# Kernel optimization log

Measured on AMD Instinct MI355X. Metric: run time of the kernel, lower is better.

The kernel has to match this reference:

```python
import jax, jax.numpy as jnp
import numpy as np

N_LAYERS, H, D, DH = 4, 16, 1024, 64
V_FR, V_EN = 32000, 32000
L_FR, L_EN, B = 513, 512, 2


def _pos_enc(x):
    # x: [L, B, D]; pe[i,j] = sin(i/10000^(j/D)) if j even else cos(i/10000^((j-1)/D))
    L, _, D_ = x.shape
    pos = jnp.arange(L, dtype=jnp.float32)[:, None]
    j = jnp.arange(D_)
    ang = pos / jnp.power(10000.0, (j - (j % 2)).astype(jnp.float32) / D_)
    pe = jnp.where(j % 2 == 0, jnp.sin(ang), jnp.cos(ang))
    return x + pe[:, None, :]


def _ln(x, g, b):
    mu = jnp.mean(x, -1, keepdims=True)
    var = jnp.mean((x - mu) ** 2, -1, keepdims=True)
    return (x - mu) * jax.lax.rsqrt(var + 1e-5) * g + b


def _mha(q_in, k_in, v_in, w, bias, causal):
    # w: [3, H, D, dh], bias: [3, H, dh]
    dh = w.shape[-1]
    Q = jnp.einsum('bld,hde->bhle', q_in, w[0]) + bias[0][None, :, None, :]
    K = jnp.einsum('bmd,hde->bhme', k_in, w[1]) + bias[1][None, :, None, :]
    V = jnp.einsum('bmd,hde->bhme', v_in, w[2]) + bias[2][None, :, None, :]
    s = jnp.einsum('bhle,bhme->bhlm', Q, K) / jnp.sqrt(jnp.float32(dh))
    if causal:
        m = jnp.tril(jnp.ones((s.shape[-2], s.shape[-1]), bool))
        s = jnp.where(m, s, -jnp.inf)
    a = jax.nn.softmax(s, axis=-1)
    o = jnp.einsum('bhlm,bhme->bhle', a, V)
    b_, h_, l_, dh_ = o.shape
    return o.transpose(0, 2, 1, 3).reshape(b_, l_, h_ * dh_)


def setup_inputs() -> dict:
    key = jax.random.key(0)
    ks = jax.random.split(key, 24)
    s = 0.02
    rn = lambda k, shp: jax.random.normal(k, shp, jnp.float32) * s
    return {
        'fr': jax.random.randint(ks[0], (L_FR, B), 0, V_FR),
        'en': jax.random.randint(ks[1], (L_EN, B), 0, V_EN),
        'emb_fr': rn(ks[2], (V_FR, D)),
        'emb_en': rn(ks[3], (V_EN, D)),
        'enc_qkv_w': rn(ks[4], (N_LAYERS, 3, H, D, DH)),
        'enc_qkv_b': rn(ks[5], (N_LAYERS, 3, H, DH)),
        'enc_fc1_w': rn(ks[6], (N_LAYERS, D, D)),
        'enc_fc1_b': rn(ks[7], (N_LAYERS, D)),
        'enc_fc2_w': rn(ks[8], (N_LAYERS, D, D)),
        'enc_fc2_b': rn(ks[9], (N_LAYERS, D)),
        'enc_ln_g': jnp.ones((N_LAYERS, 2, D)) + rn(ks[10], (N_LAYERS, 2, D)),
        'enc_ln_b': rn(ks[11], (N_LAYERS, 2, D)),
        'dec_self_qkv_w': rn(ks[12], (N_LAYERS, 3, H, D, DH)),
        'dec_self_qkv_b': rn(ks[13], (N_LAYERS, 3, H, DH)),
        'dec_cross_qkv_w': rn(ks[14], (N_LAYERS, 3, H, D, DH)),
        'dec_cross_qkv_b': rn(ks[15], (N_LAYERS, 3, H, DH)),
        'dec_fc1_w': rn(ks[16], (N_LAYERS, D, D)),
        'dec_fc1_b': rn(ks[17], (N_LAYERS, D)),
        'dec_fc2_w': rn(ks[18], (N_LAYERS, D, D)),
        'dec_fc2_b': rn(ks[19], (N_LAYERS, D)),
        'dec_ln_g': jnp.ones((N_LAYERS, 3, D)) + rn(ks[20], (N_LAYERS, 3, D)),
        'dec_ln_b': rn(ks[21], (N_LAYERS, 3, D)),
        'out_w': rn(ks[22], (D, V_EN)),
        'out_b': rn(ks[23], (V_EN,)),
    }


def reference(fr, en, emb_fr, emb_en, enc_qkv_w, enc_qkv_b, enc_fc1_w, enc_fc1_b,
              enc_fc2_w, enc_fc2_b, enc_ln_g, enc_ln_b, dec_self_qkv_w,
              dec_self_qkv_b, dec_cross_qkv_w, dec_cross_qkv_b, dec_fc1_w,
              dec_fc1_b, dec_fc2_w, dec_fc2_b, dec_ln_g, dec_ln_b, out_w, out_b):
    # Encoder (dropout p=0 -> identity in eval math)
    x = _pos_enc(emb_fr[fr[1:]]).transpose(1, 0, 2)  # [B, L_src, D]
    for n in range(N_LAYERS):
        a = _mha(x, x, x, enc_qkv_w[n], enc_qkv_b[n], causal=False)
        x = _ln(x + a, enc_ln_g[n, 0], enc_ln_b[n, 0])
        h = jnp.maximum(x @ enc_fc1_w[n] + enc_fc1_b[n], 0.0) @ enc_fc2_w[n] + enc_fc2_b[n]
        x = _ln(x + h, enc_ln_g[n, 1], enc_ln_b[n, 1])
    enc_out = x
    # Decoder
    y = _pos_enc(emb_en[en]).transpose(1, 0, 2)  # [B, L_tgt, D]
    for n in range(N_LAYERS):
        a = _mha(y, y, y, dec_self_qkv_w[n], dec_self_qkv_b[n], causal=True)
        y = _ln(y + a, dec_ln_g[n, 0], dec_ln_b[n, 0])
        c = _mha(y, enc_out, enc_out, dec_cross_qkv_w[n], dec_cross_qkv_b[n], causal=False)
        y = _ln(y + c, dec_ln_g[n, 1], dec_ln_b[n, 1])
        h = jnp.maximum(y @ dec_fc1_w[n] + dec_fc1_b[n], 0.0) @ dec_fc2_w[n] + dec_fc2_b[n]
        y = _ln(y + h, dec_ln_g[n, 2], dec_ln_b[n, 2])
    return y @ out_w + out_b  # [B, L_tgt, V_EN]
```

## Files before the change

kernel.cpp:

```cpp
#include <hip/hip_runtime.h>
#include <stdint.h>
#include <stddef.h>

typedef unsigned short u16;
typedef __attribute__((ext_vector_type(8))) short bf16x8;
typedef __attribute__((ext_vector_type(4))) float f32x4;

#define DEV __device__ __forceinline__

DEV float b2f(u16 u) { union { float f; uint32_t i; } v; v.i = ((uint32_t)u) << 16; return v.f; }
DEV u16 f2b(float f) {
  uint32_t x = __float_as_uint(f);
  x += 0x7fffu + ((x >> 16) & 1u);
  return (u16)(x >> 16);
}
DEV bf16x8 ld8f(const float* f) {
  float4 a = *(const float4*)f;
  float4 b = *(const float4*)(f + 4);
  bf16x8 r;
  ((u16*)&r)[0] = f2b(a.x); ((u16*)&r)[1] = f2b(a.y);
  ((u16*)&r)[2] = f2b(a.z); ((u16*)&r)[3] = f2b(a.w);
  ((u16*)&r)[4] = f2b(b.x); ((u16*)&r)[5] = f2b(b.y);
  ((u16*)&r)[6] = f2b(b.z); ((u16*)&r)[7] = f2b(b.w);
  return r;
}
DEV void gload16(const u16* g, u16* l) {
  __builtin_amdgcn_global_load_lds((const __attribute__((address_space(1))) void*)g,
                                   (__attribute__((address_space(3))) void*)l, 16, 0, 0);
}
DEV f32x4 mfma16(bf16x8 a, bf16x8 b, f32x4 c) {
  return __builtin_amdgcn_mfma_f32_16x16x32_bf16(a, b, c, 0, 0, 0);
}

__global__ __launch_bounds__(256) void transpose_w(const float* __restrict__ src,
                                                   u16* __restrict__ dst, int K, int N) {
  __shared__ u16 t[32][33];
  int tx = threadIdx.x, ty = threadIdx.y;
  int k0 = blockIdx.x * 32, n0 = blockIdx.y * 32;
  size_t base = (size_t)blockIdx.z * K * N;
#pragma unroll
  for (int i = 0; i < 4; i++) {
    int k = ty + 8 * i;
    t[k][tx] = f2b(src[base + (size_t)(k0 + k) * N + n0 + tx]);
  }
  __syncthreads();
#pragma unroll
  for (int i = 0; i < 4; i++) {
    int n = ty + 8 * i;
    dst[base + (size_t)(n0 + n) * K + k0 + tx] = t[tx][n];
  }
}

__global__ __launch_bounds__(256) void embed_k(const int* __restrict__ tok, const float* __restrict__ emb,
                                               float* __restrict__ o32, u16* __restrict__ ob, int shift) {
  int row = blockIdx.x;
  int b = row >> 9, l = row & 511;
  int tk = tok[(size_t)(l + shift) * 2 + b];
  const float* e = emb + (size_t)tk * 1024;
  const float c0 = -9.210340371976184f / 1024.f;
#pragma unroll
  for (int i = 0; i < 4; i++) {
    int d = threadIdx.x + i * 256;
    int j2 = d & ~1;
    float ang = (float)l * expf(c0 * (float)j2);
    float pe = (d & 1) ? cosf(ang) : sinf(ang);
    float rv = e[d] + pe;
    o32[(size_t)row * 1024 + d] = rv;
    ob[(size_t)row * 1024 + d] = f2b(rv);
  }
}

__global__ __launch_bounds__(256) void ln_k(const float* d,
                                            const float* __restrict__ g, const float* __restrict__ bb,
                                            float* o32, u16* __restrict__ ob) {
  int row = blockIdx.x;
  int tid = threadIdx.x;
  const float4 dv = ((const float4*)(d + (size_t)row * 1024))[tid];
  float v[4] = {dv.x, dv.y, dv.z, dv.w};
  float s = 0.f, s2 = 0.f;
#pragma unroll
  for (int i = 0; i < 4; i++) { s += v[i]; s2 += v[i] * v[i]; }
#pragma unroll
  for (int off = 1; off < 64; off <<= 1) {
    s += __shfl_xor(s, off);
    s2 += __shfl_xor(s2, off);
  }
  __shared__ float red[8];
  int wid = tid >> 6;
  if ((tid & 63) == 0) { red[wid * 2] = s; red[wid * 2 + 1] = s2; }
  __syncthreads();
  s = red[0] + red[2] + red[4] + red[6];
  s2 = red[1] + red[3] + red[5] + red[7];
  float mu = s * (1.f / 1024.f);
  float var = s2 * (1.f / 1024.f) - mu * mu;
  float inv = rsqrtf(var + 1e-5f);
  const float4 gv = ((const float4*)g)[tid];
  const float4 bv = ((const float4*)bb)[tid];
  float4 ov;
  ov.x = (v[0] - mu) * inv * gv.x + bv.x;
  ov.y = (v[1] - mu) * inv * gv.y + bv.y;
  ov.z = (v[2] - mu) * inv * gv.z + bv.z;
  ov.w = (v[3] - mu) * inv * gv.w + bv.w;
  ((float4*)(o32 + (size_t)row * 1024))[tid] = ov;
  uint2 p;
  p.x = (uint32_t)f2b(ov.x) | ((uint32_t)f2b(ov.y) << 16);
  p.y = (uint32_t)f2b(ov.z) | ((uint32_t)f2b(ov.w) << 16);
  ((uint2*)(ob + (size_t)row * 1024))[tid] = p;
}

template <bool RELU>
__global__ __launch_bounds__(256) void gemm_fc(const u16* __restrict__ A, const u16* __restrict__ BT,
                                               const float* __restrict__ bias,
                                               const float* __restrict__ resid, void* __restrict__ out,
                                               int N, int K) {
  __shared__ __align__(16) u16 lA[2][64 * 32];
  __shared__ __align__(16) u16 lB[2][64 * 32];
  int bx = blockIdx.x, by = blockIdx.y;
  int tid = threadIdx.x, lane = tid & 63, wid = tid >> 6;
  int l15 = lane & 15, lg = lane >> 4;
  int bm = by * 64, bn = bx * 64;
  int wr = (wid >> 1) * 32, wc = (wid & 1) * 32;
  f32x4 acc[2][2] = {};
  int r_s = tid >> 2, c_s = tid & 3;
  for (int kt = 0; kt < K; kt += 64) {
    __syncthreads();
#pragma unroll
    for (int s = 0; s < 2; s++) {
      gload16(A + (size_t)(bm + r_s) * K + kt + s * 32 + c_s * 8, &lA[s][(size_t)(wid * 64) * 8]);
      gload16(BT + (size_t)(bn + r_s) * K + kt + s * 32 + c_s * 8, &lB[s][(size_t)(wid * 64) * 8]);
    }
    __syncthreads();
#pragma unroll
    for (int s = 0; s < 2; s++) {
      bf16x8 af[2], bf_[2];
#pragma unroll
      for (int m = 0; m < 2; m++) af[m] = *(const bf16x8*)&lA[s][(wr + m * 16 + l15) * 32 + lg * 8];
#pragma unroll
      for (int n = 0; n < 2; n++) bf_[n] = *(const bf16x8*)&lB[s][(wc + n * 16 + l15) * 32 + lg * 8];
#pragma unroll
      for (int m = 0; m < 2; m++)
#pragma unroll
        for (int n = 0; n < 2; n++) acc[m][n] = mfma16(af[m], bf_[n], acc[m][n]);
    }
  }
#pragma unroll
  for (int n = 0; n < 2; n++) {
    int col = bn + wc + n * 16 + l15;
    float bv = bias[col];
#pragma unroll
    for (int m = 0; m < 2; m++) {
#pragma unroll
      for (int r = 0; r < 4; r++) {
        int row = bm + wr + m * 16 + lg * 4 + r;
        float v = acc[m][n][r] + bv;
        if (RELU) ((u16*)out)[(size_t)row * N + col] = f2b(fmaxf(v, 0.f));
        else ((float*)out)[(size_t)row * N + col] = v + resid[(size_t)row * N + col];
      }
    }
  }
}

__global__ __launch_bounds__(256) void gemm_qkv3(const u16* __restrict__ Aq, const u16* __restrict__ Akv,
                                                 const u16* __restrict__ WT, const float* __restrict__ bias,
                                                 u16* __restrict__ Qo, u16* __restrict__ Ko,
                                                 u16* __restrict__ Vto) {
  __shared__ __align__(16) u16 lA[2][64 * 32];
  __shared__ __align__(16) u16 lB[2][64 * 32];
  int bx = blockIdx.x, by = blockIdx.y;
  int t = bx >> 4;
  const u16* A = (t == 0) ? Aq : Akv;
  int tid = threadIdx.x, lane = tid & 63, wid = tid >> 6;
  int l15 = lane & 15, lg = lane >> 4;
  int bm = by * 64, bn = bx * 64;
  int wr = (wid >> 1) * 32, wc = (wid & 1) * 32;
  f32x4 acc[2][2] = {};
  int r_s = tid >> 2, c_s = tid & 3;
  for (int kt = 0; kt < 1024; kt += 64) {
    __syncthreads();
#pragma unroll
    for (int s = 0; s < 2; s++) {
      gload16(A + (size_t)(bm + r_s) * 1024 + kt + s * 32 + c_s * 8, &lA[s][(size_t)(wid * 64) * 8]);
      gload16(WT + (size_t)(bn + r_s) * 1024 + kt + s * 32 + c_s * 8, &lB[s][(size_t)(wid * 64) * 8]);
    }
    __syncthreads();
#pragma unroll
    for (int s = 0; s < 2; s++) {
      bf16x8 af[2], bf_[2];
#pragma unroll
      for (int m = 0; m < 2; m++) af[m] = *(const bf16x8*)&lA[s][(wr + m * 16 + l15) * 32 + lg * 8];
#pragma unroll
      for (int n = 0; n < 2; n++) bf_[n] = *(const bf16x8*)&lB[s][(wc + n * 16 + l15) * 32 + lg * 8];
#pragma unroll
      for (int m = 0; m < 2; m++)
#pragma unroll
        for (int n = 0; n < 2; n++) acc[m][n] = mfma16(af[m], bf_[n], acc[m][n]);
    }
  }
#pragma unroll
  for (int n = 0; n < 2; n++) {
    int col = bn + wc + n * 16 + l15;
    int h = (col >> 6) & 15, e = col & 63;
    float bv = bias[col];
#pragma unroll
    for (int m = 0; m < 2; m++) {
#pragma unroll
      for (int r = 0; r < 4; r++) {
        int row = bm + wr + m * 16 + lg * 4 + r;
        int b = row >> 9, l = row & 511;
        u16 vbv = f2b(acc[m][n][r] + bv);
        size_t bhead = (size_t)b * 16 + h;
        if (t == 0) Qo[(bhead * 512 + l) * 64 + e] = vbv;
        else if (t == 1) Ko[(bhead * 512 + l) * 64 + e] = vbv;
        else Vto[(bhead * 64 + e) * 512 + l] = vbv;
      }
    }
  }
}

template <int BM, int BN, int RS, int RM>
__global__ __launch_bounds__(256) void gemm_p3(const u16* __restrict__ A, const u16* __restrict__ BT,
                                               const float* __restrict__ bias, float* __restrict__ out,
                                               int N, int K) {
  constexpr int FM = BM / 32, FN = BN / 32;
  constexpr int L = BM / 64 + BN / 64;
  __shared__ __align__(16) u16 lA[3][BM * 32];
  __shared__ __align__(16) u16 lB[3][BN * 32];
  int b = blockIdx.x;
  int p = (b & 7) + 8 * (b >> RS);
  if (p >= N / BN) return;
  int bx = p, by = (b >> 3) & RM;
  int tid = threadIdx.x, lane = tid & 63, wid = tid >> 6;
  int l15 = lane & 15, lg = lane >> 4;
  int bm = by * BM, bn = bx * BN;
  int wr = (wid >> 1) * (BM / 2), wc = (wid & 1) * (BN / 2);
  f32x4 acc[FM][FN] = {};
  int r_s = tid >> 2, c_s = tid & 3;
  auto stage = [&](int buf, int kt) {
#pragma unroll
    for (int i = 0; i < BM / 64; i++)
      gload16(A + (size_t)(bm + i * 64 + r_s) * K + kt + c_s * 8, &lA[buf][(i * 256 + wid * 64) * 8]);
#pragma unroll
    for (int i = 0; i < BN / 64; i++)
      gload16(BT + (size_t)(bn + i * 64 + r_s) * K + kt + c_s * 8, &lB[buf][(i * 256 + wid * 64) * 8]);
  };
  int nt = K >> 5;
  stage(0, 0);
  stage(1, 32);
  asm volatile("s_waitcnt vmcnt(%0)" ::"n"(L) : "memory");
  __builtin_amdgcn_s_barrier();
  int cur = 0;
  for (int t = 0; t < nt; t++) {
    if (t + 2 < nt) stage(cur == 0 ? 2 : cur - 1, (t + 2) * 32);
    bf16x8 af[FM], bf_[FN];
#pragma unroll
    for (int m = 0; m < FM; m++) af[m] = *(const bf16x8*)&lA[cur][(wr + m * 16 + l15) * 32 + lg * 8];
#pragma unroll
    for (int n = 0; n < FN; n++) bf_[n] = *(const bf16x8*)&lB[cur][(wc + n * 16 + l15) * 32 + lg * 8];
#pragma unroll
    for (int m = 0; m < FM; m++)
#pragma unroll
      for (int n = 0; n < FN; n++) acc[m][n] = mfma16(af[m], bf_[n], acc[m][n]);
    if (t + 2 < nt) {
      asm volatile("s_waitcnt vmcnt(%0)" ::"n"(L) : "memory");
    } else if (t + 1 < nt) {
      asm volatile("s_waitcnt vmcnt(0)" ::: "memory");
    }
    if (t + 1 < nt) __builtin_amdgcn_s_barrier();
    cur = (cur == 2) ? 0 : cur + 1;
  }
#pragma unroll
  for (int n = 0; n < FN; n++) {
    int col = bn + wc + n * 16 + l15;
    float bv = bias[col];
#pragma unroll
    for (int m = 0; m < FM; m++) {
#pragma unroll
      for (int r = 0; r < 4; r++) {
        int row = bm + wr + m * 16 + lg * 4 + r;
        out[(size_t)row * N + col] = acc[m][n][r] + bv;
      }
    }
  }
}

__global__ __launch_bounds__(256) void gemm_bn(const u16* __restrict__ A, const float* __restrict__ B,
                                               const float* __restrict__ bias, float* __restrict__ out,
                                               int N, int K) {
  __shared__ __align__(16) u16 lA[128 * 32];
  __shared__ __align__(16) u16 lBn[32 * 128];
  int b = blockIdx.x;
  int p = (b & 7) + 8 * (b >> 6);
  if (p >= N / 128) return;
  int by = (b >> 3) & 7;
  int tid = threadIdx.x, lane = tid & 63;
  int wid = tid >> 6;
  int l15 = lane & 15, lg = lane >> 4;
  int bm = by * 128, bn = p * 128;
  int wr = (wid >> 1) * 64, wc = (wid & 1) * 64;
  f32x4 acc[4][4] = {};
  int r_s = tid >> 2, c_s = tid & 3;
  int br = tid >> 4, bc = tid & 15;
  for (int kt = 0; kt < K; kt += 32) {
    bf16x8 va[2], vb[2];
#pragma unroll
    for (int it = 0; it < 2; it++) {
      va[it] = *(const bf16x8*)&A[(size_t)(bm + it * 64 + r_s) * K + kt + c_s * 8];
      vb[it] = ld8f(B + (size_t)(kt + it * 16 + br) * N + bn + bc * 8);
    }
    __syncthreads();
#pragma unroll
    for (int it = 0; it < 2; it++) {
      *(bf16x8*)&lA[(size_t)(it * 256 + tid) * 8] = va[it];
      *(bf16x8*)&lBn[(size_t)(it * 256 + tid) * 8] = vb[it];
    }
    __syncthreads();
    bf16x8 af[4], bfr[4];
#pragma unroll
    for (int m = 0; m < 4; m++) af[m] = *(const bf16x8*)&lA[(wr + m * 16 + l15) * 32 + lg * 8];
#pragma unroll
    for (int n = 0; n < 4; n++) {
#pragma unroll
      for (int j = 0; j < 8; j++)
        ((short*)&bfr[n])[j] = (short)lBn[(lg * 8 + j) * 128 + wc + n * 16 + l15];
    }
#pragma unroll
    for (int m = 0; m < 4; m++)
#pragma unroll
      for (int n = 0; n < 4; n++) acc[m][n] = mfma16(af[m], bfr[n], acc[m][n]);
  }
#pragma unroll
  for (int n = 0; n < 4; n++) {
    int col = bn + wc + n * 16 + l15;
    float bv = bias[col];
#pragma unroll
    for (int m = 0; m < 4; m++) {
#pragma unroll
      for (int r = 0; r < 4; r++) {
        int row = bm + wr + m * 16 + lg * 4 + r;
        out[(size_t)row * N + col] = acc[m][n][r] + bv;
      }
    }
  }
}

template <bool CAUSAL>
__global__ __launch_bounds__(256) void attn_k(const u16* __restrict__ Qb, const u16* __restrict__ Kb,
                                              const u16* __restrict__ Vtb, const float* __restrict__ R,
                                              float* __restrict__ Ob) {
  int bh = blockIdx.y;
  int tid = threadIdx.x, lane = tid & 63, w = tid >> 6;
  int l15 = lane & 15, lg = lane >> 4;
  int q0 = blockIdx.x * 64 + w * 16;
  const u16* Qh = Qb + (size_t)bh * 512 * 64;
  const u16* Kh = Kb + (size_t)bh * 512 * 64;
  const u16* Vh = Vtb + (size_t)bh * 64 * 512;
  __shared__ __align__(16) u16 P[4][16 * 40];
  u16* Pw = &P[w][0];
  bf16x8 qa0 = *(const bf16x8*)&Qh[(size_t)(q0 + l15) * 64 + lg * 8];
  bf16x8 qa1 = *(const bf16x8*)&Qh[(size_t)(q0 + l15) * 64 + 32 + lg * 8];
  f32x4 acc[4];
#pragma unroll
  for (int c = 0; c < 4; c++) acc[c] = (f32x4){0.f, 0.f, 0.f, 0.f};
  float ls[4] = {0.f, 0.f, 0.f, 0.f};
  int ktend = CAUSAL ? ((q0 + 15) >> 5) : 15;
  for (int kt = 0; kt <= ktend; kt++) {
    int kv = kt * 32;
    f32x4 z = (f32x4){0.f, 0.f, 0.f, 0.f};
    bf16x8 k00 = *(const bf16x8*)&Kh[(size_t)(kv + l15) * 64 + lg * 8];
    bf16x8 k01 = *(const bf16x8*)&Kh[(size_t)(kv + l15) * 64 + 32 + lg * 8];
    f32x4 s0 = mfma16(qa0, k00, z);
    s0 = mfma16(qa1, k01, s0);
    bf16x8 k10 = *(const bf16x8*)&Kh[(size_t)(kv + 16 + l15) * 64 + lg * 8];
    bf16x8 k11 = *(const bf16x8*)&Kh[(size_t)(kv + 16 + l15) * 64 + 32 + lg * 8];
    f32x4 s1 = mfma16(qa0, k10, z);
    s1 = mfma16(qa1, k11, s1);
#pragma unroll
    for (int r = 0; r < 4; r++) {
      float a0 = s0[r] * 0.125f, a1 = s1[r] * 0.125f;
      if (CAUSAL) {
        int rowg = q0 + lg * 4 + r;
        if (kv + l15 > rowg) a0 = -1e30f;
        if (kv + 16 + l15 > rowg) a1 = -1e30f;
      }
      float p0 = __expf(a0), p1 = __expf(a1);
      ls[r] += p0 + p1;
      int prow = lg * 4 + r;
      Pw[prow * 40 + l15] = f2b(p0);
      Pw[prow * 40 + 16 + l15] = f2b(p1);
    }
    bf16x8 pa = *(const bf16x8*)&Pw[l15 * 40 + lg * 8];
#pragma unroll
    for (int c = 0; c < 4; c++) {
      bf16x8 vb = *(const bf16x8*)&Vh[(size_t)(c * 16 + l15) * 512 + kv + lg * 8];
      acc[c] = mfma16(pa, vb, acc[c]);
    }
  }
#pragma unroll
  for (int r = 0; r < 4; r++) {
#pragma unroll
    for (int off = 1; off < 16; off <<= 1) ls[r] += __shfl_xor(ls[r], off);
  }
  int b = bh >> 4, h = bh & 15;
#pragma unroll
  for (int r = 0; r < 4; r++) {
    float inv = 1.f / ls[r];
    int rowg = q0 + lg * 4 + r;
    size_t off0 = (size_t)(b * 512 + rowg) * 1024 + h * 64;
#pragma unroll
    for (int c = 0; c < 4; c++)
      Ob[off0 + c * 16 + l15] = R[off0 + c * 16 + l15] + acc[c][r] * inv;
  }
}

extern "C" void kernel_launch(void* const* d_in, const int* in_sizes, int n_in,
                              void* d_out, int out_size, void* d_ws, size_t ws_size,
                              hipStream_t stream) {
  const int* fr = (const int*)d_in[0];
  const int* en = (const int*)d_in[1];
  const float* emb_fr = (const float*)d_in[2];
  const float* emb_en = (const float*)d_in[3];
  const float* enc_qkv_w = (const float*)d_in[4];
  const float* enc_qkv_b = (const float*)d_in[5];
  const float* enc_fc1_w = (const float*)d_in[6];
  const float* enc_fc1_b = (const float*)d_in[7];
  const float* enc_fc2_w = (const float*)d_in[8];
  const float* enc_fc2_b = (const float*)d_in[9];
  const float* enc_ln_g = (const float*)d_in[10];
  const float* enc_ln_bb = (const float*)d_in[11];
  const float* dec_self_qkv_w = (const float*)d_in[12];
  const float* dec_self_qkv_b = (const float*)d_in[13];
  const float* dec_cross_qkv_w = (const float*)d_in[14];
  const float* dec_cross_qkv_b = (const float*)d_in[15];
  const float* dec_fc1_w = (const float*)d_in[16];
  const float* dec_fc1_b = (const float*)d_in[17];
  const float* dec_fc2_w = (const float*)d_in[18];
  const float* dec_fc2_b = (const float*)d_in[19];
  const float* dec_ln_g = (const float*)d_in[20];
  const float* dec_ln_bb = (const float*)d_in[21];
  const float* out_w = (const float*)d_in[22];
  const float* out_b = (const float*)d_in[23];

  char* o8 = (char*)d_out;
  u16* qkvT_d = (u16*)o8;
  u16* fcT_d = (u16*)(o8 + 6291456);
  float* x32 = (float*)(o8 + 8388608);
  float* y32 = (float*)(o8 + 12582912);
  float* d32 = (float*)(o8 + 16777216);
  u16* xb = (u16*)(o8 + 20971520);
  u16* hb = (u16*)(o8 + 23068672);
  u16* Qb = (u16*)(o8 + 25165824);
  u16* Kb = (u16*)(o8 + 27262976);
  u16* Vtb = (u16*)(o8 + 29360128);

  char* w8 = (char*)d_ws;
  u16* yb = (u16*)w8;
  u16* outwT = (u16*)(w8 + 2097152);
  u16* eqkvT = (u16*)(w8 + 67633152);
  u16* dsqkvT = (u16*)(w8 + 92798976);
  u16* dcqkvT = (u16*)(w8 + 117964800);
  u16* efc1T = (u16*)(w8 + 143130624);
  u16* efc2T = (u16*)(w8 + 151519232);
  u16* dfc1T = (u16*)(w8 + 159907840);
  u16* dfc2T = (u16*)(w8 + 168296448);
  int tier = (ws_size >= 176685056u) ? 2 : (ws_size >= 67633152u) ? 1 : 0;

  dim3 tb(32, 8);
  if (tier >= 1)
    transpose_w<<<dim3(32, 1000, 1), tb, 0, stream>>>(out_w, outwT, 1024, 32000);
  if (tier == 2) {
    transpose_w<<<dim3(32, 2, 192), tb, 0, stream>>>(enc_qkv_w, eqkvT, 1024, 64);
    transpose_w<<<dim3(32, 2, 192), tb, 0, stream>>>(dec_self_qkv_w, dsqkvT, 1024, 64);
    transpose_w<<<dim3(32, 2, 192), tb, 0, stream>>>(dec_cross_qkv_w, dcqkvT, 1024, 64);
    transpose_w<<<dim3(32, 32, 4), tb, 0, stream>>>(enc_fc1_w, efc1T, 1024, 1024);
    transpose_w<<<dim3(32, 32, 4), tb, 0, stream>>>(enc_fc2_w, efc2T, 1024, 1024);
    transpose_w<<<dim3(32, 32, 4), tb, 0, stream>>>(dec_fc1_w, dfc1T, 1024, 1024);
    transpose_w<<<dim3(32, 32, 4), tb, 0, stream>>>(dec_fc2_w, dfc2T, 1024, 1024);
  }

  embed_k<<<1024, 256, 0, stream>>>(fr, emb_fr, x32, xb, 1);
  embed_k<<<1024, 256, 0, stream>>>(en, emb_en, y32, yb, 0);

  for (int n = 0; n < 4; n++) {
    const u16* wqkv;
    if (tier == 2) wqkv = eqkvT + (size_t)n * 3145728;
    else {
      transpose_w<<<dim3(32, 2, 48), tb, 0, stream>>>(enc_qkv_w + (size_t)n * 48 * 65536, qkvT_d, 1024, 64);
      wqkv = qkvT_d;
    }
    gemm_qkv3<<<dim3(48, 16), 256, 0, stream>>>(xb, xb, wqkv, enc_qkv_b + (size_t)n * 3072, Qb, Kb, Vtb);
    attn_k<false><<<dim3(8, 32), 256, 0, stream>>>(Qb, Kb, Vtb, x32, d32);
    ln_k<<<1024, 256, 0, stream>>>(d32, enc_ln_g + (size_t)(n * 2) * 1024,
                                   enc_ln_bb + (size_t)(n * 2) * 1024, x32, xb);
    const u16* w1;
    if (tier == 2) w1 = efc1T + (size_t)n * 1048576;
    else {
      transpose_w<<<dim3(32, 32, 1), tb, 0, stream>>>(enc_fc1_w + (size_t)n * 1048576, fcT_d, 1024, 1024);
      w1 = fcT_d;
    }
    gemm_fc<true><<<dim3(16, 16), 256, 0, stream>>>(xb, w1, enc_fc1_b + (size_t)n * 1024,
                                                    nullptr, hb, 1024, 1024);
    const u16* w2;
    if (tier == 2) w2 = efc2T + (size_t)n * 1048576;
    else {
      transpose_w<<<dim3(32, 32, 1), tb, 0, stream>>>(enc_fc2_w + (size_t)n * 1048576, fcT_d, 1024, 1024);
      w2 = fcT_d;
    }
    gemm_fc<false><<<dim3(16, 16), 256, 0, stream>>>(hb, w2, enc_fc2_b + (size_t)n * 1024,
                                                     x32, d32, 1024, 1024);
    ln_k<<<1024, 256, 0, stream>>>(d32, enc_ln_g + (size_t)(n * 2 + 1) * 1024,
                                   enc_ln_bb + (size_t)(n * 2 + 1) * 1024, x32, xb);
  }
  for (int n = 0; n < 4; n++) {
    const u16* wq;
    if (tier == 2) wq = dsqkvT + (size_t)n * 3145728;
    else {
      transpose_w<<<dim3(32, 2, 48), tb, 0, stream>>>(dec_self_qkv_w + (size_t)n * 48 * 65536, qkvT_d, 1024, 64);
      wq = qkvT_d;
    }
    gemm_qkv3<<<dim3(48, 16), 256, 0, stream>>>(yb, yb, wq, dec_self_qkv_b + (size_t)n * 3072, Qb, Kb, Vtb);
    attn_k<true><<<dim3(8, 32), 256, 0, stream>>>(Qb, Kb, Vtb, y32, d32);
    ln_k<<<1024, 256, 0, stream>>>(d32, dec_ln_g + (size_t)(n * 3) * 1024,
                                   dec_ln_bb + (size_t)(n * 3) * 1024, y32, yb);
    if (tier == 2) wq = dcqkvT + (size_t)n * 3145728;
    else {
      transpose_w<<<dim3(32, 2, 48), tb, 0, stream>>>(dec_cross_qkv_w + (size_t)n * 48 * 65536, qkvT_d, 1024, 64);
      wq = qkvT_d;
    }
    gemm_qkv3<<<dim3(48, 16), 256, 0, stream>>>(yb, xb, wq, dec_cross_qkv_b + (size_t)n * 3072, Qb, Kb, Vtb);
    attn_k<false><<<dim3(8, 32), 256, 0, stream>>>(Qb, Kb, Vtb, y32, d32);
    ln_k<<<1024, 256, 0, stream>>>(d32, dec_ln_g + (size_t)(n * 3 + 1) * 1024,
                                   dec_ln_bb + (size_t)(n * 3 + 1) * 1024, y32, yb);
    const u16* w1;
    if (tier == 2) w1 = dfc1T + (size_t)n * 1048576;
    else {
      transpose_w<<<dim3(32, 32, 1), tb, 0, stream>>>(dec_fc1_w + (size_t)n * 1048576, fcT_d, 1024, 1024);
      w1 = fcT_d;
    }
    gemm_fc<true><<<dim3(16, 16), 256, 0, stream>>>(yb, w1, dec_fc1_b + (size_t)n * 1024,
                                                    nullptr, hb, 1024, 1024);
    const u16* w2;
    if (tier == 2) w2 = dfc2T + (size_t)n * 1048576;
    else {
      transpose_w<<<dim3(32, 32, 1), tb, 0, stream>>>(dec_fc2_w + (size_t)n * 1048576, fcT_d, 1024, 1024);
      w2 = fcT_d;
    }
    gemm_fc<false><<<dim3(16, 16), 256, 0, stream>>>(hb, w2, dec_fc2_b + (size_t)n * 1024,
                                                     y32, d32, 1024, 1024);
    ln_k<<<1024, 256, 0, stream>>>(d32, dec_ln_g + (size_t)(n * 3 + 2) * 1024,
                                   dec_ln_bb + (size_t)(n * 3 + 2) * 1024, y32, yb);
  }
  if (tier >= 1)
    gemm_p3<128, 128, 6, 7><<<dim3(2048), 256, 0, stream>>>(yb, outwT, out_b, (float*)d_out, 32000, 1024);
  else
    gemm_bn<<<dim3(2048), 256, 0, stream>>>(yb, out_w, out_b, (float*)d_out, 32000, 1024);
}
```

Measured before the change: 991.0 us.

## Double-buffer GEMM LDS loads, prefetch K in attention, merge weight transposes

The fc and qkv GEMMs now double-buffer their LDS tiles and issue the next K-tile's async loads before computing the current one, waiting with vmcnt and raw barriers in place of two syncthreads per iteration. This is meant to hide global-load latency behind the MFMA work. The attention kernel prefetches the next K block into registers. The seven per-weight transpose launches collapse into two batched kernels, relying on the workspace buffers being contiguous. Shared memory use doubles, which may lower occupancy, and the vmcnt(4) count must match the number of outstanding loads per stage.

```diff
diff --git a/kernel.cpp b/kernel.cpp
--- a/kernel.cpp
+++ b/kernel.cpp
@@ -48,6 +48,56 @@
   for (int i = 0; i < 4; i++) {
     int n = ty + 8 * i;
     dst[base + (size_t)(n0 + n) * K + k0 + tx] = t[tx][n];
+  }
+}
+
+__global__ __launch_bounds__(256) void transpose_qkvT(const float* __restrict__ s0,
+                                                      const float* __restrict__ s1,
+                                                      const float* __restrict__ s2,
+                                                      u16* __restrict__ dst) {
+  int z = blockIdx.z;
+  const float* src = (z < 192) ? s0 : (z < 384) ? s1 : s2;
+  int zi = (z < 192) ? z : (z < 384) ? z - 192 : z - 384;
+  size_t sbase = (size_t)zi * 65536;
+  size_t dbase = (size_t)z * 65536;
+  __shared__ u16 t[32][33];
+  int tx = threadIdx.x, ty = threadIdx.y;
+  int k0 = blockIdx.x * 32, n0 = blockIdx.y * 32;
+#pragma unroll
+  for (int i = 0; i < 4; i++) {
+    int k = ty + 8 * i;
+    t[k][tx] = f2b(src[sbase + (size_t)(k0 + k) * 64 + n0 + tx]);
+  }
+  __syncthreads();
+#pragma unroll
+  for (int i = 0; i < 4; i++) {
+    int n = ty + 8 * i;
+    dst[dbase + (size_t)(n0 + n) * 1024 + k0 + tx] = t[tx][n];
+  }
+}
+
+__global__ __launch_bounds__(256) void transpose_fcT(const float* __restrict__ s0,
+                                                     const float* __restrict__ s1,
+                                                     const float* __restrict__ s2,
+                                                     const float* __restrict__ s3,
+                                                     u16* __restrict__ dst) {
+  int z = blockIdx.z;
+  const float* src = (z < 4) ? s0 : (z < 8) ? s1 : (z < 12) ? s2 : s3;
+  size_t sbase = (size_t)(z & 3) * 1048576;
+  size_t dbase = (size_t)z * 1048576;
+  __shared__ u16 t[32][33];
+  int tx = threadIdx.x, ty = threadIdx.y;
+  int k0 = blockIdx.x * 32, n0 = blockIdx.y * 32;
+#pragma unroll
+  for (int i = 0; i < 4; i++) {
+    int k = ty + 8 * i;
+    t[k][tx] = f2b(src[sbase + (size_t)(k0 + k) * 1024 + n0 + tx]);
+  }
+  __syncthreads();
+#pragma unroll
+  for (int i = 0; i < 4; i++) {
+    int n = ty + 8 * i;
+    dst[dbase + (size_t)(n0 + n) * 1024 + k0 + tx] = t[tx][n];
   }
 }
 
@@ -113,8 +163,8 @@
                                                const float* __restrict__ bias,
                                                const float* __restrict__ resid, void* __restrict__ out,
                                                int N, int K) {
-  __shared__ __align__(16) u16 lA[2][64 * 32];
-  __shared__ __align__(16) u16 lB[2][64 * 32];
+  __shared__ __align__(16) u16 lA[2][2][64 * 32];
+  __shared__ __align__(16) u16 lB[2][2][64 * 32];
   int bx = blockIdx.x, by = blockIdx.y;
   int tid = threadIdx.x, lane = tid & 63, wid = tid >> 6;
   int l15 = lane & 15, lg = lane >> 4;
@@ -122,26 +172,38 @@
   int wr = (wid >> 1) * 32, wc = (wid & 1) * 32;
   f32x4 acc[2][2] = {};
   int r_s = tid >> 2, c_s = tid & 3;
-  for (int kt = 0; kt < K; kt += 64) {
-    __syncthreads();
+  auto stage = [&](int pp, int kt) {
 #pragma unroll
     for (int s = 0; s < 2; s++) {
-      gload16(A + (size_t)(bm + r_s) * K + kt + s * 32 + c_s * 8, &lA[s][(size_t)(wid * 64) * 8]);
-      gload16(BT + (size_t)(bn + r_s) * K + kt + s * 32 + c_s * 8, &lB[s][(size_t)(wid * 64) * 8]);
-    }
-    __syncthreads();
+      gload16(A + (size_t)(bm + r_s) * K + kt + s * 32 + c_s * 8, &lA[pp][s][(size_t)(wid * 64) * 8]);
+      gload16(BT + (size_t)(bn + r_s) * K + kt + s * 32 + c_s * 8, &lB[pp][s][(size_t)(wid * 64) * 8]);
+    }
+  };
+  int nt = K >> 6;
+  stage(0, 0);
+  int pp = 0;
+  for (int t = 0; t < nt; t++) {
+    if (t + 1 < nt) {
+      stage(pp ^ 1, (t + 1) * 64);
+      asm volatile("s_waitcnt vmcnt(4)" ::: "memory");
+    } else {
+      asm volatile("s_waitcnt vmcnt(0)" ::: "memory");
+    }
+    __builtin_amdgcn_s_barrier();
 #pragma unroll
     for (int s = 0; s < 2; s++) {
       bf16x8 af[2], bf_[2];
 #pragma unroll
-      for (int m = 0; m < 2; m++) af[m] = *(const bf16x8*)&lA[s][(wr + m * 16 + l15) * 32 + lg * 8];
-#pragma unroll
-      for (int n = 0; n < 2; n++) bf_[n] = *(const bf16x8*)&lB[s][(wc + n * 16 + l15) * 32 + lg * 8];
+      for (int m = 0; m < 2; m++) af[m] = *(const bf16x8*)&lA[pp][s][(wr + m * 16 + l15) * 32 + lg * 8];
+#pragma unroll
+      for (int n = 0; n < 2; n++) bf_[n] = *(const bf16x8*)&lB[pp][s][(wc + n * 16 + l15) * 32 + lg * 8];
 #pragma unroll
       for (int m = 0; m < 2; m++)
 #pragma unroll
         for (int n = 0; n < 2; n++) acc[m][n] = mfma16(af[m], bf_[n], acc[m][n]);
     }
+    __builtin_amdgcn_s_barrier();
+    pp ^= 1;
   }
 #pragma unroll
   for (int n = 0; n < 2; n++) {
@@ -164,37 +226,48 @@
                                                  const u16* __restrict__ WT, const float* __restrict__ bias,
                                                  u16* __restrict__ Qo, u16* __restrict__ Ko,
                                                  u16* __restrict__ Vto) {
-  __shared__ __align__(16) u16 lA[2][64 * 32];
-  __shared__ __align__(16) u16 lB[2][64 * 32];
+  __shared__ __align__(16) u16 lA[2][2][64 * 32];
+  __shared__ __align__(16) u16 lB[2][2][64 * 32];
   int bx = blockIdx.x, by = blockIdx.y;
-  int t = bx >> 4;
-  const u16* A = (t == 0) ? Aq : Akv;
+  int t_ = bx >> 4;
+  const u16* A = (t_ == 0) ? Aq : Akv;
   int tid = threadIdx.x, lane = tid & 63, wid = tid >> 6;
   int l15 = lane & 15, lg = lane >> 4;
   int bm = by * 64, bn = bx * 64;
   int wr = (wid >> 1) * 32, wc = (wid & 1) * 32;
   f32x4 acc[2][2] = {};
   int r_s = tid >> 2, c_s = tid & 3;
-  for (int kt = 0; kt < 1024; kt += 64) {
-    __syncthreads();
+  auto stage = [&](int pp, int kt) {
 #pragma unroll
     for (int s = 0; s < 2; s++) {
-      gload16(A + (size_t)(bm + r_s) * 1024 + kt + s * 32 + c_s * 8, &lA[s][(size_t)(wid * 64) * 8]);
-      gload16(WT + (size_t)(bn + r_s) * 1024 + kt + s * 32 + c_s * 8, &lB[s][(size_t)(wid * 64) * 8]);
-    }
-    __syncthreads();
+      gload16(A + (size_t)(bm + r_s) * 1024 + kt + s * 32 + c_s * 8, &lA[pp][s][(size_t)(wid * 64) * 8]);
+      gload16(WT + (size_t)(bn + r_s) * 1024 + kt + s * 32 + c_s * 8, &lB[pp][s][(size_t)(wid * 64) * 8]);
+    }
+  };
+  stage(0, 0);
+  int pp = 0;
+  for (int t = 0; t < 16; t++) {
+    if (t + 1 < 16) {
+      stage(pp ^ 1, (t + 1) * 64);
+      asm volatile("s_waitcnt vmcnt(4)" ::: "memory");
+    } else {
+      asm volatile("s_waitcnt vmcnt(0)" ::: "memory");
+    }
+    __builtin_amdgcn_s_barrier();
 #pragma unroll
     for (int s = 0; s < 2; s++) {
       bf16x8 af[2], bf_[2];
 #pragma unroll
-      for (int m = 0; m < 2; m++) af[m] = *(const bf16x8*)&lA[s][(wr + m * 16 + l15) * 32 + lg * 8];
-#pragma unroll
-      for (int n = 0; n < 2; n++) bf_[n] = *(const bf16x8*)&lB[s][(wc + n * 16 + l15) * 32 + lg * 8];
+      for (int m = 0; m < 2; m++) af[m] = *(const bf16x8*)&lA[pp][s][(wr + m * 16 + l15) * 32 + lg * 8];
+#pragma unroll
+      for (int n = 0; n < 2; n++) bf_[n] = *(const bf16x8*)&lB[pp][s][(wc + n * 16 + l15) * 32 + lg * 8];
 #pragma unroll
       for (int m = 0; m < 2; m++)
 #pragma unroll
         for (int n = 0; n < 2; n++) acc[m][n] = mfma16(af[m], bf_[n], acc[m][n]);
     }
+    __builtin_amdgcn_s_barrier();
+    pp ^= 1;
   }
 #pragma unroll
   for (int n = 0; n < 2; n++) {
@@ -209,8 +282,8 @@
         int b = row >> 9, l = row & 511;
         u16 vbv = f2b(acc[m][n][r] + bv);
         size_t bhead = (size_t)b * 16 + h;
-        if (t == 0) Qo[(bhead * 512 + l) * 64 + e] = vbv;
-        else if (t == 1) Ko[(bhead * 512 + l) * 64 + e] = vbv;
+        if (t_ == 0) Qo[(bhead * 512 + l) * 64 + e] = vbv;
+        else if (t_ == 1) Ko[(bhead * 512 + l) * 64 + e] = vbv;
         else Vto[(bhead * 64 + e) * 512 + l] = vbv;
       }
     }
@@ -363,17 +436,25 @@
   for (int c = 0; c < 4; c++) acc[c] = (f32x4){0.f, 0.f, 0.f, 0.f};
   float ls[4] = {0.f, 0.f, 0.f, 0.f};
   int ktend = CAUSAL ? ((q0 + 15) >> 5) : 15;
+  bf16x8 kn00 = *(const bf16x8*)&Kh[(size_t)(l15) * 64 + lg * 8];
+  bf16x8 kn01 = *(const bf16x8*)&Kh[(size_t)(l15) * 64 + 32 + lg * 8];
+  bf16x8 kn10 = *(const bf16x8*)&Kh[(size_t)(16 + l15) * 64 + lg * 8];
+  bf16x8 kn11 = *(const bf16x8*)&Kh[(size_t)(16 + l15) * 64 + 32 + lg * 8];
   for (int kt = 0; kt <= ktend; kt++) {
     int kv = kt * 32;
+    bf16x8 c00 = kn00, c01 = kn01, c10 = kn10, c11 = kn11;
+    if (kt < ktend) {
+      int kv2 = kv + 32;
+      kn00 = *(const bf16x8*)&Kh[(size_t)(kv2 + l15) * 64 + lg * 8];
+      kn01 = *(const bf16x8*)&Kh[(size_t)(kv2 + l15) * 64 + 32 + lg * 8];
+      kn10 = *(const bf16x8*)&Kh[(size_t)(kv2 + 16 + l15) * 64 + lg * 8];
+      kn11 = *(const bf16x8*)&Kh[(size_t)(kv2 + 16 + l15) * 64 + 32 + lg * 8];
+    }
     f32x4 z = (f32x4){0.f, 0.f, 0.f, 0.f};
-    bf16x8 k00 = *(const bf16x8*)&Kh[(size_t)(kv + l15) * 64 + lg * 8];
-    bf16x8 k01 = *(const bf16x8*)&Kh[(size_t)(kv + l15) * 64 + 32 + lg * 8];
-    f32x4 s0 = mfma16(qa0, k00, z);
-    s0 = mfma16(qa1, k01, s0);
-    bf16x8 k10 = *(const bf16x8*)&Kh[(size_t)(kv + 16 + l15) * 64 + lg * 8];
-    bf16x8 k11 = *(const bf16x8*)&Kh[(size_t)(kv + 16 + l15) * 64 + 32 + lg * 8];
-    f32x4 s1 = mfma16(qa0, k10, z);
-    s1 = mfma16(qa1, k11, s1);
+    f32x4 s0 = mfma16(qa0, c00, z);
+    s0 = mfma16(qa1, c01, s0);
+    f32x4 s1 = mfma16(qa0, c10, z);
+    s1 = mfma16(qa1, c11, s1);
 #pragma unroll
     for (int r = 0; r < 4; r++) {
       float a0 = s0[r] * 0.125f, a1 = s1[r] * 0.125f;
@@ -468,13 +549,8 @@
   if (tier >= 1)
     transpose_w<<<dim3(32, 1000, 1), tb, 0, stream>>>(out_w, outwT, 1024, 32000);
   if (tier == 2) {
-    transpose_w<<<dim3(32, 2, 192), tb, 0, stream>>>(enc_qkv_w, eqkvT, 1024, 64);
-    transpose_w<<<dim3(32, 2, 192), tb, 0, stream>>>(dec_self_qkv_w, dsqkvT, 1024, 64);
-    transpose_w<<<dim3(32, 2, 192), tb, 0, stream>>>(dec_cross_qkv_w, dcqkvT, 1024, 64);
-    transpose_w<<<dim3(32, 32, 4), tb, 0, stream>>>(enc_fc1_w, efc1T, 1024, 1024);
-    transpose_w<<<dim3(32, 32, 4), tb, 0, stream>>>(enc_fc2_w, efc2T, 1024, 1024);
-    transpose_w<<<dim3(32, 32, 4), tb, 0, stream>>>(dec_fc1_w, dfc1T, 1024, 1024);
-    transpose_w<<<dim3(32, 32, 4), tb, 0, stream>>>(dec_fc2_w, dfc2T, 1024, 1024);
+    transpose_qkvT<<<dim3(32, 2, 576), tb, 0, stream>>>(enc_qkv_w, dec_self_qkv_w, dec_cross_qkv_w, eqkvT);
+    transpose_fcT<<<dim3(32, 32, 16), tb, 0, stream>>>(enc_fc1_w, enc_fc2_w, dec_fc1_w, dec_fc2_w, efc1T);
   }
 
   embed_k<<<1024, 256, 0, stream>>>(fr, emb_fr, x32, xb, 1);
```

New measurement: 956.0 us. 1.04x faster.
